# Kernel optimization log

Hardware: AMD Instinct MI355X
Metric: run time of the kernel (lower is better)

The kernel has to match this reference:

```python
import jax, jax.numpy as jnp
import numpy as np

B, S, D, H = 2, 2048, 1024, 16
MASK_VAL = -50000.0

def setup_inputs() -> dict:
    key = jax.random.key(0)
    k1, k2, k3, k4 = jax.random.split(key, 4)
    # weights stored as [in, out] so projection is x @ W (equals torch Linear with W.T)
    s = 1.0 / np.sqrt(D)
    return {
        "x": jax.random.normal(k1, (B, S, D), dtype=jnp.float32),
        "Wq": jax.random.normal(k2, (D, D), dtype=jnp.float32) * s,
        "Wkv": jax.random.normal(k3, (D, 2 * D), dtype=jnp.float32) * s,
        "Wo": jax.random.normal(k4, (D, D), dtype=jnp.float32) * s,
    }

def reference(x, Wq, Wkv, Wo):
    b, sl, d = x.shape
    h = H
    hd = d // h
    scale = hd ** (-0.5)
    q = x @ Wq                      # [b, sl, d]
    kv = x @ Wkv                    # [b, sl, 2d]
    k, v = jnp.split(kv, 2, axis=-1)
    # [b, h, s, hd]
    q = q.reshape(b, sl, h, hd).transpose(0, 2, 1, 3)
    k = k.reshape(b, sl, h, hd).transpose(0, 2, 1, 3)
    v = v.reshape(b, sl, h, hd).transpose(0, 2, 1, 3)
    dots = jnp.einsum('bhid,bhjd->bhij', q * scale, k)  # [b,h,s,s]
    # causal: strictly-upper-triangular entries set to MASK_VAL
    causal = jnp.tril(jnp.ones((sl, sl), dtype=bool))
    dots = jnp.where(causal, dots, MASK_VAL)
    attn = jax.nn.softmax(dots, axis=-1)
    out = jnp.einsum('bhij,bhjd->bihd', attn, v).reshape(b, sl, d)
    return out @ Wo
```

## Files before the change

### kernel.cpp

```cpp
#include <hip/hip_runtime.h>

typedef __bf16 bf16_t;
typedef unsigned short u16;
typedef __attribute__((ext_vector_type(8))) __bf16 bf16x8;
typedef __attribute__((ext_vector_type(4))) float f32x4;
typedef __attribute__((ext_vector_type(4))) u16 u16x4;
typedef __attribute__((ext_vector_type(8))) u16 u16x8;

#define SS 2048
#define PSTR 72

__device__ __forceinline__ u16 f2b(float f) {
    return __builtin_bit_cast(u16, (__bf16)f);
}

__device__ __forceinline__ float fexp2(float x) {
#if __has_builtin(__builtin_amdgcn_exp2f)
    return __builtin_amdgcn_exp2f(x);
#else
    float r;
    asm("v_exp_f32 %0, %1" : "=v"(r) : "v"(x));
    return r;
#endif
}

__device__ __forceinline__ void async_copy16(const u16* g, u16* l) {
    __builtin_amdgcn_global_load_lds(
        (__attribute__((address_space(1))) void*)(u16*)g,
        (__attribute__((address_space(3))) void*)l, 16, 0, 0);
}

__device__ __forceinline__ bf16x8 ldfrag(const u16* p) {
    return __builtin_bit_cast(bf16x8, *(const u16x8*)p);
}

__global__ __launch_bounds__(256)
void cast_x_kernel(const float* __restrict__ x, u16* __restrict__ xb) {
    size_t i = ((size_t)blockIdx.x * 256 + threadIdx.x) * 8;
    float4 a = *(const float4*)(x + i);
    float4 b = *(const float4*)(x + i + 4);
    u16x8 o;
    o[0] = f2b(a.x); o[1] = f2b(a.y); o[2] = f2b(a.z); o[3] = f2b(a.w);
    o[4] = f2b(b.x); o[5] = f2b(b.y); o[6] = f2b(b.z); o[7] = f2b(b.w);
    *(u16x8*)(xb + i) = o;
}

__global__ __launch_bounds__(256)
void transpose_all(const float* __restrict__ Wq, const float* __restrict__ Wkv,
                   const float* __restrict__ Wo, u16* __restrict__ WcatT,
                   u16* __restrict__ WoT) {
    const int z = blockIdx.z;
    if (z != 1 && blockIdx.y >= 16) return;
    const float* src; u16* dst; int N; float scale;
    if (z == 0)      { src = Wq;  dst = WcatT;               N = 1024; scale = 0.125f * 1.44269504089f; }
    else if (z == 1) { src = Wkv; dst = WcatT + 1024 * 1024; N = 2048; scale = 1.0f; }
    else             { src = Wo;  dst = WoT;                 N = 1024; scale = 1.0f; }
    __shared__ __attribute__((aligned(16))) u16 tile[64][72];
    const int k0 = blockIdx.x * 64, n0 = blockIdx.y * 64;
    const int tid = threadIdx.x;
#pragma unroll
    for (int p = 0; p < 4; ++p) {
        int c = p * 256 + tid;
        int r = c >> 4, c4 = c & 15;
        float4 v = *(const float4*)(src + (size_t)(k0 + r) * N + n0 + c4 * 4);
        u16x4 o;
        o[0] = f2b(v.x * scale); o[1] = f2b(v.y * scale);
        o[2] = f2b(v.z * scale); o[3] = f2b(v.w * scale);
        *(u16x4*)&tile[r][c4 * 4] = o;
    }
    __syncthreads();
#pragma unroll
    for (int p = 0; p < 4; ++p) {
        int c = p * 256 + tid;
        int n = c >> 4, k4 = c & 15;
        u16x4 o;
#pragma unroll
        for (int i = 0; i < 4; ++i) o[i] = tile[k4 * 4 + i][n];
        *(u16x4*)(dst + (size_t)(n0 + n) * 1024 + k0 + k4 * 4) = o;
    }
}

__global__ __launch_bounds__(256)
void transpose_v(const u16* __restrict__ QKV, u16* __restrict__ VTg) {
    __shared__ __attribute__((aligned(16))) u16 tile[64][72];
    const int s0 = blockIdx.x * 64;
    const int bh = blockIdx.y;
    const int b = bh >> 4, h = bh & 15;
    const int tid = threadIdx.x;
    const u16* src = QKV + ((size_t)b * SS + s0) * 3072 + 2048 + h * 64;
#pragma unroll
    for (int p = 0; p < 4; ++p) {
        int c = p * 256 + tid;
        int s = c >> 4, h4 = c & 15;
        *(u16x4*)&tile[s][h4 * 4] = *(const u16x4*)(src + (size_t)s * 3072 + h4 * 4);
    }
    __syncthreads();
    u16* dst = VTg + (size_t)bh * 64 * 2048 + s0;
#pragma unroll
    for (int p = 0; p < 4; ++p) {
        int c = p * 256 + tid;
        int hd = c >> 4, s4 = c & 15;
        u16x4 o;
#pragma unroll
        for (int i = 0; i < 4; ++i) o[i] = tile[s4 * 4 + i][hd];
        *(u16x4*)(dst + (size_t)hd * 2048 + s4 * 4) = o;
    }
}

template <typename OutT>
__global__ __launch_bounds__(256, 2)
void gemm_bt(const u16* __restrict__ A, const u16* __restrict__ BT,
             OutT* __restrict__ C, int M, int N, int K) {
    __shared__ __attribute__((aligned(16))) u16 As[128 * 32];
    __shared__ __attribute__((aligned(16))) u16 Bs[128 * 32];
    const int tid = threadIdx.x;
    const int wave = tid >> 6, lane = tid & 63;
    const int l15 = lane & 15, quad = lane >> 4;
    const int m0 = blockIdx.y * 128, n0 = blockIdx.x * 128;
    const int wm = (wave >> 1) * 64, wn = (wave & 1) * 64;
    const f32x4 zero = {0.f, 0.f, 0.f, 0.f};
    f32x4 acc[4][4];
#pragma unroll
    for (int i = 0; i < 4; ++i)
#pragma unroll
        for (int j = 0; j < 4; ++j) acc[i][j] = zero;
    const int r0 = tid >> 2, kc = (tid & 3) * 8;
    for (int k0 = 0; k0 < K; k0 += 32) {
        async_copy16(A + (size_t)(m0 + r0) * K + k0 + kc, As + tid * 8);
        async_copy16(BT + (size_t)(n0 + r0) * K + k0 + kc, Bs + tid * 8);
        async_copy16(A + (size_t)(m0 + 64 + r0) * K + k0 + kc, As + (256 + tid) * 8);
        async_copy16(BT + (size_t)(n0 + 64 + r0) * K + k0 + kc, Bs + (256 + tid) * 8);
        __syncthreads();
        bf16x8 af[4], bf[4];
#pragma unroll
        for (int t = 0; t < 4; ++t) {
            af[t] = ldfrag(As + (wm + t * 16 + l15) * 32 + quad * 8);
            bf[t] = ldfrag(Bs + (wn + t * 16 + l15) * 32 + quad * 8);
        }
#pragma unroll
        for (int mt = 0; mt < 4; ++mt)
#pragma unroll
            for (int nt = 0; nt < 4; ++nt)
                acc[mt][nt] = __builtin_amdgcn_mfma_f32_16x16x32_bf16(
                    af[mt], bf[nt], acc[mt][nt], 0, 0, 0);
        __syncthreads();
    }
#pragma unroll
    for (int mt = 0; mt < 4; ++mt)
#pragma unroll
        for (int nt = 0; nt < 4; ++nt) {
            const int n = n0 + wn + nt * 16 + l15;
#pragma unroll
            for (int r = 0; r < 4; ++r) {
                const int m = m0 + wm + mt * 16 + quad * 4 + r;
                float v = acc[mt][nt][r];
                if constexpr (sizeof(OutT) == 2) C[(size_t)m * N + n] = (OutT)f2b(v);
                else                             C[(size_t)m * N + n] = v;
            }
        }
}

__global__ __launch_bounds__(256, 2)
void gemm_bt64(const u16* __restrict__ A, const u16* __restrict__ BT,
               float* __restrict__ C, int M, int N, int K) {
    __shared__ __attribute__((aligned(16))) u16 As[128 * 32];
    __shared__ __attribute__((aligned(16))) u16 Bs[64 * 32];
    const int tid = threadIdx.x;
    const int wave = tid >> 6, lane = tid & 63;
    const int l15 = lane & 15, quad = lane >> 4;
    const int m0 = blockIdx.y * 128, n0 = blockIdx.x * 64;
    const int wm = (wave >> 1) * 64, wn = (wave & 1) * 32;
    const f32x4 zero = {0.f, 0.f, 0.f, 0.f};
    f32x4 acc[4][2];
#pragma unroll
    for (int i = 0; i < 4; ++i)
#pragma unroll
        for (int j = 0; j < 2; ++j) acc[i][j] = zero;
    const int r0 = tid >> 2, kc = (tid & 3) * 8;
    for (int k0 = 0; k0 < K; k0 += 32) {
        async_copy16(A + (size_t)(m0 + r0) * K + k0 + kc, As + tid * 8);
        async_copy16(A + (size_t)(m0 + 64 + r0) * K + k0 + kc, As + (256 + tid) * 8);
        async_copy16(BT + (size_t)(n0 + r0) * K + k0 + kc, Bs + tid * 8);
        __syncthreads();
        bf16x8 af[4], bf[2];
#pragma unroll
        for (int t = 0; t < 4; ++t)
            af[t] = ldfrag(As + (wm + t * 16 + l15) * 32 + quad * 8);
#pragma unroll
        for (int t = 0; t < 2; ++t)
            bf[t] = ldfrag(Bs + (wn + t * 16 + l15) * 32 + quad * 8);
#pragma unroll
        for (int mt = 0; mt < 4; ++mt)
#pragma unroll
            for (int nt = 0; nt < 2; ++nt)
                acc[mt][nt] = __builtin_amdgcn_mfma_f32_16x16x32_bf16(
                    af[mt], bf[nt], acc[mt][nt], 0, 0, 0);
        __syncthreads();
    }
#pragma unroll
    for (int mt = 0; mt < 4; ++mt)
#pragma unroll
        for (int nt = 0; nt < 2; ++nt) {
            const int n = n0 + wn + nt * 16 + l15;
#pragma unroll
            for (int r = 0; r < 4; ++r) {
                const int m = m0 + wm + mt * 16 + quad * 4 + r;
                C[(size_t)m * N + n] = acc[mt][nt][r];
            }
        }
}

__device__ __forceinline__ void attn_scoreT(
    const bf16x8 (&kf)[2], const bf16x8 (&qf)[4][2],
    float (&l_i)[4], u16* __restrict__ P, bool diag, int w16, int l15, int quad) {
    const f32x4 cinit = {-10.f, -10.f, -10.f, -10.f};
#pragma unroll
    for (int t = 0; t < 4; ++t) {
        f32x4 a = __builtin_amdgcn_mfma_f32_16x16x32_bf16(kf[0], qf[t][0], cinit, 0, 0, 0);
        f32x4 s = __builtin_amdgcn_mfma_f32_16x16x32_bf16(kf[1], qf[t][1], a, 0, 0, 0);
        if (diag) {
#pragma unroll
            for (int r = 0; r < 4; ++r)
                if (w16 + quad * 4 + r > t * 16 + l15) s[r] = -1e30f;
        }
        u16x4 pk;
        float acc = 0.f;
#pragma unroll
        for (int r = 0; r < 4; ++r) {
            float pv = fexp2(s[r]);
            acc += pv;
            pk[r] = f2b(pv);
        }
        l_i[t] += acc;
        *(u16x4*)(P + (t * 16 + l15) * PSTR + w16 + quad * 4) = pk;
    }
}

__device__ __forceinline__ void attn_pv(
    const u16* __restrict__ P, const bf16x8 (&vf)[4][2],
    f32x4 (&O)[4], int l15, int quad) {
    bf16x8 pf0 = ldfrag(P + l15 * PSTR + quad * 8);
    bf16x8 pf1 = ldfrag(P + l15 * PSTR + 32 + quad * 8);
#pragma unroll
    for (int nt = 0; nt < 4; ++nt) {
        O[nt] = __builtin_amdgcn_mfma_f32_16x16x32_bf16(pf0, vf[nt][0], O[nt], 0, 0, 0);
        O[nt] = __builtin_amdgcn_mfma_f32_16x16x32_bf16(pf1, vf[nt][1], O[nt], 0, 0, 0);
    }
}

__global__ __launch_bounds__(256, 2)
void attn_kernel(const u16* __restrict__ QKV, const u16* __restrict__ VTg,
                 u16* __restrict__ AO) {
    __shared__ __attribute__((aligned(16))) u16 Kt[2][2 * 64 * 32];
    __shared__ __attribute__((aligned(16))) u16 Vt[2][2 * 64 * 32];
    __shared__ __attribute__((aligned(16))) u16 Pq[128 * PSTR];
    const int tid = threadIdx.x;
    const int wave = tid >> 6, lane = tid & 63;
    const int l15 = lane & 15, quad = lane >> 4;
    const int w16 = wave * 16;
    const int bh = blockIdx.y, b = bh >> 4, h = bh & 15;
    const int xe = b ? 15 - (int)blockIdx.x : (int)blockIdx.x;
    const int qbA = 31 - xe, qbB = xe;
    const int qA0 = qbA * 64, qB0 = qbB * 64;
    const size_t bS = (size_t)b * SS;
    const u16* vbase = VTg + (size_t)bh * 64 * 2048;
    const int rr = (tid >> 2) & 63, kc8 = (tid & 3) * 8;

    {
        const u16* qsrcA = QKV + (bS + qA0 + rr) * 3072 + h * 64 + kc8;
        async_copy16(qsrcA,      Pq + tid * 8);
        async_copy16(qsrcA + 32, Pq + (256 + tid) * 8);
        const u16* qsrcB = QKV + (bS + qB0 + rr) * 3072 + h * 64 + kc8;
        async_copy16(qsrcB,      Pq + (512 + tid) * 8);
        async_copy16(qsrcB + 32, Pq + (768 + tid) * 8);
        const u16* ksrc = QKV + (bS + rr) * 3072 + 1024 + h * 64 + kc8;
        async_copy16(ksrc,      Kt[0] + tid * 8);
        async_copy16(ksrc + 32, Kt[0] + (256 + tid) * 8);
        const u16* vsrc = vbase + (size_t)rr * 2048 + kc8;
        async_copy16(vsrc,      Vt[0] + tid * 8);
        async_copy16(vsrc + 32, Vt[0] + (256 + tid) * 8);
    }
    __syncthreads();
    bf16x8 qfA[4][2], qfB[4][2];
#pragma unroll
    for (int t = 0; t < 4; ++t)
#pragma unroll
        for (int ks = 0; ks < 2; ++ks) {
            qfA[t][ks] = ldfrag(Pq + ks * 2048 + (t * 16 + l15) * 32 + quad * 8);
            qfB[t][ks] = ldfrag(Pq + 4096 + ks * 2048 + (t * 16 + l15) * 32 + quad * 8);
        }
    __syncthreads();

    u16* PA = Pq;
    u16* PB = Pq + 64 * PSTR;
    float lA[4], lB[4];
    f32x4 OA[4], OB[4];
    const f32x4 zero = {0.f, 0.f, 0.f, 0.f};
#pragma unroll
    for (int t = 0; t < 4; ++t) { lA[t] = lB[t] = 0.f; }
#pragma unroll
    for (int nt = 0; nt < 4; ++nt) { OA[nt] = zero; OB[nt] = zero; }

    for (int j = 0; j <= qbA; ++j) {
        if (j < qbA) {
            const int kv1 = (j + 1) * 64;
            const int nb = (j + 1) & 1;
            const u16* ksrc = QKV + (bS + kv1 + rr) * 3072 + 1024 + h * 64 + kc8;
            async_copy16(ksrc,      Kt[nb] + tid * 8);
            async_copy16(ksrc + 32, Kt[nb] + (256 + tid) * 8);
            const u16* vsrc = vbase + (size_t)rr * 2048 + kv1 + kc8;
            async_copy16(vsrc,      Vt[nb] + tid * 8);
            async_copy16(vsrc + 32, Vt[nb] + (256 + tid) * 8);
        }
        const bool bAct = (j <= qbB);
        const u16* KB = Kt[j & 1];
        const u16* VB = Vt[j & 1];
        bf16x8 kf[2];
#pragma unroll
        for (int ks = 0; ks < 2; ++ks)
            kf[ks] = ldfrag(KB + ks * 2048 + (w16 + l15) * 32 + quad * 8);
        attn_scoreT(kf, qfA, lA, PA, j == qbA, w16, l15, quad);
        if (bAct)
            attn_scoreT(kf, qfB, lB, PB, j == qbB, w16, l15, quad);
        __syncthreads();
        bf16x8 vf[4][2];
#pragma unroll
        for (int nt = 0; nt < 4; ++nt)
#pragma unroll
            for (int ks = 0; ks < 2; ++ks)
                vf[nt][ks] = ldfrag(VB + ks * 2048 + (nt * 16 + l15) * 32 + quad * 8);
        attn_pv(PA + w16 * PSTR, vf, OA, l15, quad);
        if (bAct)
            attn_pv(PB + w16 * PSTR, vf, OB, l15, quad);
        __syncthreads();
    }

    float* lsh = (float*)Kt;
#pragma unroll
    for (int t = 0; t < 4; ++t) {
        float sA = lA[t];
        sA += __shfl_xor(sA, 16); sA += __shfl_xor(sA, 32);
        float sB = lB[t];
        sB += __shfl_xor(sB, 16); sB += __shfl_xor(sB, 32);
        if (lane < 16) {
            lsh[(t * 16 + l15) * 4 + wave] = sA;
            lsh[(64 + t * 16 + l15) * 4 + wave] = sB;
        }
    }
    __syncthreads();
#pragma unroll
    for (int r = 0; r < 4; ++r) {
        const int qlA = w16 + quad * 4 + r;
        f32x4 la = *(const f32x4*)&lsh[qlA * 4];
        f32x4 lb = *(const f32x4*)&lsh[(64 + qlA) * 4];
        float invA = 1.0f / (la[0] + la[1] + la[2] + la[3]);
        float invB = 1.0f / (lb[0] + lb[1] + lb[2] + lb[3]);
        size_t rowA = bS + (size_t)qA0 + qlA;
        size_t rowB = bS + (size_t)qB0 + qlA;
#pragma unroll
        for (int nt = 0; nt < 4; ++nt) {
            AO[rowA * 1024 + h * 64 + nt * 16 + l15] = f2b(OA[nt][r] * invA);
            AO[rowB * 1024 + h * 64 + nt * 16 + l15] = f2b(OB[nt][r] * invB);
        }
    }
}

extern "C" void kernel_launch(void* const* d_in, const int* in_sizes, int n_in,
                              void* d_out, int out_size, void* d_ws, size_t ws_size,
                              hipStream_t stream) {
    (void)in_sizes; (void)n_in; (void)out_size; (void)ws_size;
    const float* x   = (const float*)d_in[0];
    const float* Wq  = (const float*)d_in[1];
    const float* Wkv = (const float*)d_in[2];
    const float* Wo  = (const float*)d_in[3];
    float* out = (float*)d_out;
    char* ws = (char*)d_ws;
    u16* xb    = (u16*)(ws);
    u16* WcatT = (u16*)(ws + (size_t)(8 << 20));
    u16* WoT   = (u16*)(ws + (size_t)(14 << 20));
    u16* QKV   = (u16*)(ws + (size_t)(16 << 20));
    u16* VTb   = (u16*)(ws + (size_t)(40 << 20));
    u16* AO    = xb;

    cast_x_kernel<<<2048, 256, 0, stream>>>(x, xb);
    transpose_all<<<dim3(16, 32, 3), 256, 0, stream>>>(Wq, Wkv, Wo, WcatT, WoT);
    gemm_bt<u16><<<dim3(24, 32), 256, 0, stream>>>(xb, WcatT, QKV, 4096, 3072, 1024);
    transpose_v<<<dim3(32, 32), 256, 0, stream>>>(QKV, VTb);
    attn_kernel<<<dim3(16, 32), 256, 0, stream>>>(QKV, VTb, AO);
    gemm_bt64<<<dim3(16, 32), 256, 0, stream>>>(AO, WoT, out, 4096, 1024, 1024);
}
```

Before: 184.7 us.

## Swizzle attention K/V/Q LDS tiles, relax barriers, and raise MFMA priority

Applies an XOR swizzle to the 16-byte column chunks of the K, V and Q shared-memory tiles, both in the global-source offset of the async copies and in the fragment reads, to cut LDS bank conflicts. The mid-loop __syncthreads is replaced by a barrier that waits only on LDS counters, so outstanding prefetches are not forced to complete there; the end-of-loop barrier still waits on both. It also wraps the MFMA sequences in s_setprio to favour matrix issue across waves. The swizzle must match exactly between the copy and the read side, and the hand-written waitcnt barriers depend on the compiler not reordering memory operations across them.

```diff
diff --git a/kernel.cpp b/kernel.cpp
--- a/kernel.cpp
+++ b/kernel.cpp
@@ -33,6 +33,22 @@
 __device__ __forceinline__ bf16x8 ldfrag(const u16* p) {
     return __builtin_bit_cast(bf16x8, *(const u16x8*)p);
 }
+
+__device__ __forceinline__ const u16* swzp(const u16* base, int row, int quad) {
+    return base + row * 32 + ((quad ^ ((row >> 1) & 3)) * 8);
+}
+
+#define BAR_LGKM() do {                                     \
+    asm volatile("s_waitcnt lgkmcnt(0)" ::: "memory");      \
+    __builtin_amdgcn_s_barrier();                           \
+    asm volatile("" ::: "memory");                          \
+} while (0)
+
+#define BAR_VM_LGKM() do {                                  \
+    asm volatile("s_waitcnt vmcnt(0) lgkmcnt(0)" ::: "memory"); \
+    __builtin_amdgcn_s_barrier();                           \
+    asm volatile("" ::: "memory");                          \
+} while (0)
 
 __global__ __launch_bounds__(256)
 void cast_x_kernel(const float* __restrict__ x, u16* __restrict__ xb) {
@@ -216,8 +232,10 @@
     const f32x4 cinit = {-10.f, -10.f, -10.f, -10.f};
 #pragma unroll
     for (int t = 0; t < 4; ++t) {
+        __builtin_amdgcn_s_setprio(1);
         f32x4 a = __builtin_amdgcn_mfma_f32_16x16x32_bf16(kf[0], qf[t][0], cinit, 0, 0, 0);
         f32x4 s = __builtin_amdgcn_mfma_f32_16x16x32_bf16(kf[1], qf[t][1], a, 0, 0, 0);
+        __builtin_amdgcn_s_setprio(0);
         if (diag) {
 #pragma unroll
             for (int r = 0; r < 4; ++r)
@@ -241,11 +259,13 @@
     f32x4 (&O)[4], int l15, int quad) {
     bf16x8 pf0 = ldfrag(P + l15 * PSTR + quad * 8);
     bf16x8 pf1 = ldfrag(P + l15 * PSTR + 32 + quad * 8);
+    __builtin_amdgcn_s_setprio(1);
 #pragma unroll
     for (int nt = 0; nt < 4; ++nt) {
         O[nt] = __builtin_amdgcn_mfma_f32_16x16x32_bf16(pf0, vf[nt][0], O[nt], 0, 0, 0);
         O[nt] = __builtin_amdgcn_mfma_f32_16x16x32_bf16(pf1, vf[nt][1], O[nt], 0, 0, 0);
     }
+    __builtin_amdgcn_s_setprio(0);
 }
 
 __global__ __launch_bounds__(256, 2)
@@ -264,19 +284,20 @@
     const int qA0 = qbA * 64, qB0 = qbB * 64;
     const size_t bS = (size_t)b * SS;
     const u16* vbase = VTg + (size_t)bh * 64 * 2048;
-    const int rr = (tid >> 2) & 63, kc8 = (tid & 3) * 8;
+    const int rr = (tid >> 2) & 63;
+    const int kcs = (((tid & 3) ^ ((tid >> 3) & 3)) * 8);
 
     {
-        const u16* qsrcA = QKV + (bS + qA0 + rr) * 3072 + h * 64 + kc8;
+        const u16* qsrcA = QKV + (bS + qA0 + rr) * 3072 + h * 64 + kcs;
         async_copy16(qsrcA,      Pq + tid * 8);
         async_copy16(qsrcA + 32, Pq + (256 + tid) * 8);
-        const u16* qsrcB = QKV + (bS + qB0 + rr) * 3072 + h * 64 + kc8;
+        const u16* qsrcB = QKV + (bS + qB0 + rr) * 3072 + h * 64 + kcs;
         async_copy16(qsrcB,      Pq + (512 + tid) * 8);
         async_copy16(qsrcB + 32, Pq + (768 + tid) * 8);
-        const u16* ksrc = QKV + (bS + rr) * 3072 + 1024 + h * 64 + kc8;
+        const u16* ksrc = QKV + (bS + rr) * 3072 + 1024 + h * 64 + kcs;
         async_copy16(ksrc,      Kt[0] + tid * 8);
         async_copy16(ksrc + 32, Kt[0] + (256 + tid) * 8);
-        const u16* vsrc = vbase + (size_t)rr * 2048 + kc8;
+        const u16* vsrc = vbase + (size_t)rr * 2048 + kcs;
         async_copy16(vsrc,      Vt[0] + tid * 8);
         async_copy16(vsrc + 32, Vt[0] + (256 + tid) * 8);
     }
@@ -286,8 +307,8 @@
     for (int t = 0; t < 4; ++t)
 #pragma unroll
         for (int ks = 0; ks < 2; ++ks) {
-            qfA[t][ks] = ldfrag(Pq + ks * 2048 + (t * 16 + l15) * 32 + quad * 8);
-            qfB[t][ks] = ldfrag(Pq + 4096 + ks * 2048 + (t * 16 + l15) * 32 + quad * 8);
+            qfA[t][ks] = ldfrag(swzp(Pq + ks * 2048, t * 16 + l15, quad));
+            qfB[t][ks] = ldfrag(swzp(Pq + 4096 + ks * 2048, t * 16 + l15, quad));
         }
     __syncthreads();
 
@@ -305,10 +326,10 @@
         if (j < qbA) {
             const int kv1 = (j + 1) * 64;
             const int nb = (j + 1) & 1;
-            const u16* ksrc = QKV + (bS + kv1 + rr) * 3072 + 1024 + h * 64 + kc8;
+            const u16* ksrc = QKV + (bS + kv1 + rr) * 3072 + 1024 + h * 64 + kcs;
             async_copy16(ksrc,      Kt[nb] + tid * 8);
             async_copy16(ksrc + 32, Kt[nb] + (256 + tid) * 8);
-            const u16* vsrc = vbase + (size_t)rr * 2048 + kv1 + kc8;
+            const u16* vsrc = vbase + (size_t)rr * 2048 + kv1 + kcs;
             async_copy16(vsrc,      Vt[nb] + tid * 8);
             async_copy16(vsrc + 32, Vt[nb] + (256 + tid) * 8);
         }
@@ -318,21 +339,21 @@
         bf16x8 kf[2];
 #pragma unroll
         for (int ks = 0; ks < 2; ++ks)
-            kf[ks] = ldfrag(KB + ks * 2048 + (w16 + l15) * 32 + quad * 8);
+            kf[ks] = ldfrag(swzp(KB + ks * 2048, w16 + l15, quad));
         attn_scoreT(kf, qfA, lA, PA, j == qbA, w16, l15, quad);
         if (bAct)
             attn_scoreT(kf, qfB, lB, PB, j == qbB, w16, l15, quad);
-        __syncthreads();
+        BAR_LGKM();
         bf16x8 vf[4][2];
 #pragma unroll
         for (int nt = 0; nt < 4; ++nt)
 #pragma unroll
             for (int ks = 0; ks < 2; ++ks)
-                vf[nt][ks] = ldfrag(VB + ks * 2048 + (nt * 16 + l15) * 32 + quad * 8);
+                vf[nt][ks] = ldfrag(swzp(VB + ks * 2048, nt * 16 + l15, quad));
         attn_pv(PA + w16 * PSTR, vf, OA, l15, quad);
         if (bAct)
             attn_pv(PB + w16 * PSTR, vf, OB, l15, quad);
-        __syncthreads();
+        BAR_VM_LGKM();
     }
 
     float* lsh = (float*)Kt;
```

New measurement: 186.8 us. Within noise of the previous version (+1.2%).

## Double-buffer LDS tiles in projection GEMMs to overlap loads with MFMA

Applied to the files above, without the earlier changes.

Both GEMM kernels now hold two shared-memory tile buffers. Each kernel issues the async global-to-LDS copy for the next K-slice before running the MFMA work on the current slice, so memory latency can overlap with compute instead of stalling at the barrier. The main gemm_bt kernel also raises its launch-bounds occupancy hint from 2 to 3 blocks per CU. The cost is twice the LDS per block, and the tighter occupancy hint may increase register pressure or cause spilling.

```diff
diff --git a/kernel.cpp b/kernel.cpp
--- a/kernel.cpp
+++ b/kernel.cpp
@@ -108,11 +108,11 @@
 }
 
 template <typename OutT>
-__global__ __launch_bounds__(256, 2)
+__global__ __launch_bounds__(256, 3)
 void gemm_bt(const u16* __restrict__ A, const u16* __restrict__ BT,
              OutT* __restrict__ C, int M, int N, int K) {
-    __shared__ __attribute__((aligned(16))) u16 As[128 * 32];
-    __shared__ __attribute__((aligned(16))) u16 Bs[128 * 32];
+    __shared__ __attribute__((aligned(16))) u16 As[2][128 * 32];
+    __shared__ __attribute__((aligned(16))) u16 Bs[2][128 * 32];
     const int tid = threadIdx.x;
     const int wave = tid >> 6, lane = tid & 63;
     const int l15 = lane & 15, quad = lane >> 4;
@@ -125,17 +125,24 @@
 #pragma unroll
         for (int j = 0; j < 4; ++j) acc[i][j] = zero;
     const int r0 = tid >> 2, kc = (tid & 3) * 8;
-    for (int k0 = 0; k0 < K; k0 += 32) {
-        async_copy16(A + (size_t)(m0 + r0) * K + k0 + kc, As + tid * 8);
-        async_copy16(BT + (size_t)(n0 + r0) * K + k0 + kc, Bs + tid * 8);
-        async_copy16(A + (size_t)(m0 + 64 + r0) * K + k0 + kc, As + (256 + tid) * 8);
-        async_copy16(BT + (size_t)(n0 + 64 + r0) * K + k0 + kc, Bs + (256 + tid) * 8);
-        __syncthreads();
+    auto stage = [&](int bsel, int k0) {
+        async_copy16(A + (size_t)(m0 + r0) * K + k0 + kc, As[bsel] + tid * 8);
+        async_copy16(BT + (size_t)(n0 + r0) * K + k0 + kc, Bs[bsel] + tid * 8);
+        async_copy16(A + (size_t)(m0 + 64 + r0) * K + k0 + kc, As[bsel] + (256 + tid) * 8);
+        async_copy16(BT + (size_t)(n0 + 64 + r0) * K + k0 + kc, Bs[bsel] + (256 + tid) * 8);
+    };
+    stage(0, 0);
+    __syncthreads();
+    const int nk = K >> 5;
+    for (int t = 0; t < nk; ++t) {
+        if (t + 1 < nk) stage((t + 1) & 1, (t + 1) * 32);
+        const u16* Ab = As[t & 1];
+        const u16* Bb = Bs[t & 1];
         bf16x8 af[4], bf[4];
 #pragma unroll
-        for (int t = 0; t < 4; ++t) {
-            af[t] = ldfrag(As + (wm + t * 16 + l15) * 32 + quad * 8);
-            bf[t] = ldfrag(Bs + (wn + t * 16 + l15) * 32 + quad * 8);
+        for (int s = 0; s < 4; ++s) {
+            af[s] = ldfrag(Ab + (wm + s * 16 + l15) * 32 + quad * 8);
+            bf[s] = ldfrag(Bb + (wn + s * 16 + l15) * 32 + quad * 8);
         }
 #pragma unroll
         for (int mt = 0; mt < 4; ++mt)
@@ -163,8 +170,8 @@
 __global__ __launch_bounds__(256, 2)
 void gemm_bt64(const u16* __restrict__ A, const u16* __restrict__ BT,
                float* __restrict__ C, int M, int N, int K) {
-    __shared__ __attribute__((aligned(16))) u16 As[128 * 32];
-    __shared__ __attribute__((aligned(16))) u16 Bs[64 * 32];
+    __shared__ __attribute__((aligned(16))) u16 As[2][128 * 32];
+    __shared__ __attribute__((aligned(16))) u16 Bs[2][64 * 32];
     const int tid = threadIdx.x;
     const int wave = tid >> 6, lane = tid & 63;
     const int l15 = lane & 15, quad = lane >> 4;
@@ -177,18 +184,25 @@
 #pragma unroll
         for (int j = 0; j < 2; ++j) acc[i][j] = zero;
     const int r0 = tid >> 2, kc = (tid & 3) * 8;
-    for (int k0 = 0; k0 < K; k0 += 32) {
-        async_copy16(A + (size_t)(m0 + r0) * K + k0 + kc, As + tid * 8);
-        async_copy16(A + (size_t)(m0 + 64 + r0) * K + k0 + kc, As + (256 + tid) * 8);
-        async_copy16(BT + (size_t)(n0 + r0) * K + k0 + kc, Bs + tid * 8);
-        __syncthreads();
+    auto stage = [&](int bsel, int k0) {
+        async_copy16(A + (size_t)(m0 + r0) * K + k0 + kc, As[bsel] + tid * 8);
+        async_copy16(A + (size_t)(m0 + 64 + r0) * K + k0 + kc, As[bsel] + (256 + tid) * 8);
+        async_copy16(BT + (size_t)(n0 + r0) * K + k0 + kc, Bs[bsel] + tid * 8);
+    };
+    stage(0, 0);
+    __syncthreads();
+    const int nk = K >> 5;
+    for (int t = 0; t < nk; ++t) {
+        if (t + 1 < nk) stage((t + 1) & 1, (t + 1) * 32);
+        const u16* Ab = As[t & 1];
+        const u16* Bb = Bs[t & 1];
         bf16x8 af[4], bf[2];
 #pragma unroll
-        for (int t = 0; t < 4; ++t)
-            af[t] = ldfrag(As + (wm + t * 16 + l15) * 32 + quad * 8);
-#pragma unroll
-        for (int t = 0; t < 2; ++t)
-            bf[t] = ldfrag(Bs + (wn + t * 16 + l15) * 32 + quad * 8);
+        for (int s = 0; s < 4; ++s)
+            af[s] = ldfrag(Ab + (wm + s * 16 + l15) * 32 + quad * 8);
+#pragma unroll
+        for (int s = 0; s < 2; ++s)
+            bf[s] = ldfrag(Bb + (wn + s * 16 + l15) * 32 + quad * 8);
 #pragma unroll
         for (int mt = 0; mt < 4; ++mt)
 #pragma unroll
```

Measured after the change: 184.6 us. Within noise of the previous version (-0.0%).
